# Kernel tuning notes

Hardware: AMD Instinct MI355X
Metric: run time of the kernel (lower is better)

The kernel has to match this reference:

```python
import jax, jax.numpy as jnp
import numpy as np

S, IN_DIM = 16384, 1024
NUM_PROJ, PROJ_DIM, BINS = 100, 64, 20
D = NUM_PROJ * PROJ_DIM
EPS = 1e-12  # F.normalize eps


def setup_inputs() -> dict:
    key = jax.random.key(0)
    kx, kw = jax.random.split(key)
    x = jax.random.normal(kx, (S, IN_DIM), dtype=jnp.float32)
    W = jax.random.normal(kw, (D, IN_DIM), dtype=jnp.float32)  # nn.Linear weight, std=1.0 init
    # mins/maxs as produced by cal_min_max over the data (per projected dim)
    proj = x @ W.T
    mins = jnp.min(proj, axis=0)
    maxs = jnp.max(proj, axis=0)
    return {"x": x, "W": W, "mins": mins, "maxs": maxs,
            "num_of_projection": NUM_PROJ, "bins": BINS}


def reference(x, W, mins, maxs, num_of_projection, bins):
    # get_global_feature(x, normalize=True), all histograms fused via scatter-add
    proj = x @ W.T                                   # [S, D]
    d = proj.shape[1]
    proj_dim = d // num_of_projection
    width = maxs - mins                              # [D]
    # torch.histc semantics: values in [min, max] counted; value == max -> last bin
    idx = jnp.floor((proj - mins) / width * bins).astype(jnp.int32)
    idx = jnp.clip(idx, 0, bins - 1)
    valid = (proj >= mins) & (proj <= maxs)
    flat = idx + jnp.arange(d, dtype=jnp.int32)[None, :] * bins   # [S, D]
    hist = jnp.zeros(d * bins, dtype=proj.dtype).at[flat.reshape(-1)].add(
        valid.reshape(-1).astype(proj.dtype))
    gv = hist.reshape(num_of_projection, proj_dim, bins)
    # F.normalize(p=2, dim=2)
    norm = jnp.linalg.norm(gv, axis=2, keepdims=True)
    gv = gv / jnp.maximum(norm, EPS)
    return gv
```

## Files before the change

### kernel.cpp

```cpp
#include <hip/hip_runtime.h>
#include <cmath>

#define S_DIM 16384
#define K_DIM 1024
#define D_DIM 6400
#define NBINS 20
#define HSTRIDE 21

using half_t = _Float16;
using half8  = __attribute__((ext_vector_type(8))) _Float16;
using f32x4  = __attribute__((ext_vector_type(4))) float;

__global__ void cvt_f32_f16(const float* __restrict__ a, half_t* __restrict__ da, int n8a,
                            const float* __restrict__ b, half_t* __restrict__ db, int n8b,
                            float4* __restrict__ z, int nz4) {
  int i = blockIdx.x * blockDim.x + threadIdx.x;
  if (i < nz4) z[i] = (float4){0.f, 0.f, 0.f, 0.f};
  const float* s; half_t* d; int idx;
  if (i < n8a) { s = a; d = da; idx = i; }
  else { idx = i - n8a; if (idx >= n8b) return; s = b; d = db; }
  float4 v0 = ((const float4*)s)[idx * 2];
  float4 v1 = ((const float4*)s)[idx * 2 + 1];
  half8 h = { (half_t)v0.x, (half_t)v0.y, (half_t)v0.z, (half_t)v0.w,
              (half_t)v1.x, (half_t)v1.y, (half_t)v1.z, (half_t)v1.w };
  ((half8*)d)[idx] = h;
}

#define VMWAIT(N) __asm__ volatile("s_waitcnt vmcnt(" #N ")" ::: "memory")
#define BAR()     __asm__ volatile("s_barrier" ::: "memory")
#define SP1()     __builtin_amdgcn_s_setprio(1)
#define SP0()     __builtin_amdgcn_s_setprio(0)

#define GLL(SRC, DST) __builtin_amdgcn_global_load_lds(                      \
    (const __attribute__((address_space(1))) void*)(SRC),                    \
    (__attribute__((address_space(3))) void*)(DST), 16, 0, 0)

__global__ __launch_bounds__(512, 2) void gemm_hist256(
    const half_t* __restrict__ xh, const half_t* __restrict__ wh,
    const float* __restrict__ mins, const float* __restrict__ maxs,
    int* __restrict__ ghist)
{
  __shared__ __align__(16) char ldsA[65536];
  __shared__ __align__(16) char ldsB[65536];
  __shared__ int shist[256 * HSTRIDE];

  const int t    = threadIdx.x;
  const int lane = t & 63;
  const int wv   = t >> 6;
  const int wm   = wv >> 2;
  const int wn   = wv & 3;
  const int l16  = lane & 15;
  const int quad = lane >> 4;

  const int bid = blockIdx.x;
  const int wg  = (bid & 7) * 200 + (bid >> 3);
  const int ct  = wg / 64;
  const int rt  = wg - ct * 64;
  const int colBase = ct * 256;
  const int rowBase = rt * 256;

  for (int i = t; i < 256 * HSTRIDE; i += 512) shist[i] = 0;

  const char* pA[2];
  const char* pB[2];
#pragma unroll
  for (int ks = 0; ks < 2; ++ks) {
    int ch = ((ks * 4 + quad) ^ (lane & 7)) * 16;
    pA[ks] = ldsA + (wm * 128 + l16) * 128 + ch;
    pB[ks] = ldsB + (wn * 64 + l16) * 128 + ch;
  }

  const int r0 = t >> 3;
  const int gOff = r0 * K_DIM + (((t & 7) ^ (r0 & 7)) * 8);
  const int wvD  = wv * 1024;

  const half_t* aS = xh + (size_t)rowBase * K_DIM + gOff;
  const half_t* bS = wh + (size_t)colBase * K_DIM + gOff;

#define STA(PB) {                                                            \
    GLL(aS,                 ldsA + (PB) + wvD);                              \
    GLL(aS +  64 * K_DIM,   ldsA + (PB) +  8192 + wvD);                      \
    GLL(aS + 128 * K_DIM,   ldsA + (PB) + 16384 + wvD);                      \
    GLL(aS + 192 * K_DIM,   ldsA + (PB) + 24576 + wvD);                      \
    aS += 64; }
#define STB(PB) {                                                            \
    GLL(bS,                 ldsB + (PB) + wvD);                              \
    GLL(bS +  64 * K_DIM,   ldsB + (PB) +  8192 + wvD);                      \
    GLL(bS + 128 * K_DIM,   ldsB + (PB) + 16384 + wvD);                      \
    GLL(bS + 192 * K_DIM,   ldsB + (PB) + 24576 + wvD);                      \
    bS += 64; }

  f32x4 acc[8][4];
#pragma unroll
  for (int m = 0; m < 8; ++m)
#pragma unroll
    for (int n = 0; n < 4; ++n) acc[m][n] = (f32x4){0.f, 0.f, 0.f, 0.f};

  half8 aLo[4][2], aHi[4][2], B0[2][2], B1[2][2];

#define LD_ALO(PB)                                                           \
  _Pragma("unroll") for (int fm = 0; fm < 4; ++fm)                           \
  _Pragma("unroll") for (int ks = 0; ks < 2; ++ks)                           \
    aLo[fm][ks] = *(const half8*)(pA[ks] + (PB) + fm * 2048);
#define LD_AHI(PB)                                                           \
  _Pragma("unroll") for (int fm = 0; fm < 4; ++fm)                           \
  _Pragma("unroll") for (int ks = 0; ks < 2; ++ks)                           \
    aHi[fm][ks] = *(const half8*)(pA[ks] + (PB) + 8192 + fm * 2048);
#define LD_B(REG, FNB, PB)                                                   \
  _Pragma("unroll") for (int fn = 0; fn < 2; ++fn)                           \
  _Pragma("unroll") for (int ks = 0; ks < 2; ++ks)                           \
    REG[fn][ks] = *(const half8*)(pB[ks] + (PB) + ((FNB) + fn) * 2048);
#define MQ(AH, BH, MOFF, NOFF)                                               \
  _Pragma("unroll") for (int fm = 0; fm < 4; ++fm)                           \
  _Pragma("unroll") for (int fn = 0; fn < 2; ++fn)                           \
  _Pragma("unroll") for (int ks = 0; ks < 2; ++ks)                           \
    acc[(MOFF) + fm][(NOFF) + fn] = __builtin_amdgcn_mfma_f32_16x16x32_f16(  \
        AH[fm][ks], BH[fn][ks], acc[(MOFF) + fm][(NOFF) + fn], 0, 0, 0);

  STA(0); STB(0); STA(32768); STB(32768);
  VMWAIT(8); BAR();
  LD_ALO(0);
  LD_B(B0, 0, 0);

#define TILE(PB, RDA, RDB, STG)                                              \
  {                                                                          \
    LD_B(B1, 2, PB);                             \
    SP1(); MQ(aLo, B0, 0, 0); SP0();             \
    LD_AHI(PB);                                  \
    SP1(); MQ(aLo, B1, 0, 2); SP0();             \
    VMWAIT(4); BAR();                            \
    if (RDA) LD_ALO((PB) ^ 32768);               \
    SP1(); MQ(aHi, B1, 4, 2); SP0();             \
    VMWAIT(0); BAR();                            \
    if (STG) { STA(PB); STB(PB); }               \
    SP1(); MQ(aHi, B0, 4, 0); SP0();             \
    if (RDB) LD_B(B0, 0, (PB) ^ 32768);          \
  }

  for (int tt = 0; tt < 12; tt += 2) {
    TILE(0,     1, 1, 1);
    TILE(32768, 1, 1, 1);
  }
  TILE(0,     1, 1, 1);
  TILE(32768, 1, 1, 1);
  TILE(0,     1, 1, 0);
  TILE(32768, 0, 0, 0);

#pragma unroll
  for (int nf = 0; nf < 4; ++nf) {
    const int lc = wn * 64 + nf * 16 + l16;
    const float a = mins[colBase + lc], b = maxs[colBase + lc];
    const float sc = (float)NBINS / (b - a);
    int* colHist = &shist[lc * HSTRIDE];
#pragma unroll
    for (int mf = 0; mf < 8; ++mf) {
#pragma unroll
      for (int r = 0; r < 4; ++r) {
        float v = acc[mf][nf][r];
        if (v >= a && v <= b) {
          int bin = (int)((v - a) * sc);
          bin = bin > NBINS - 1 ? NBINS - 1 : bin;
          atomicAdd(&colHist[bin], 1);
        }
      }
    }
  }
  __syncthreads();
  for (int i = t; i < 256 * NBINS; i += 512) {
    int col = i / NBINS, bin = i - col * NBINS;
    int v = shist[col * HSTRIDE + bin];
    if (v) atomicAdd(&ghist[colBase * NBINS + i], v);
  }
}

__global__ __launch_bounds__(256) void gemm_hist_fb(
    const float* __restrict__ xf, const float* __restrict__ wf,
    const float* __restrict__ mins, const float* __restrict__ maxs,
    int* __restrict__ ghist)
{
  __shared__ __align__(16) half_t ldsA[4096];
  __shared__ __align__(16) half_t ldsB[4096];
  __shared__ int shist[128 * HSTRIDE];

  const int t     = threadIdx.x;
  const int lane  = t & 63;
  const int wv    = t >> 6;
  const int waveM = wv >> 1;
  const int waveN = wv & 1;
  const int l16   = lane & 15;
  const int quad  = lane >> 4;
  const int colBase = blockIdx.x * 128;

  for (int i = t; i < 128 * HSTRIDE; i += 256) shist[i] = 0;

  float mn[4], mx[4], inv[4];
  int lcol[4];
#pragma unroll
  for (int nt = 0; nt < 4; ++nt) {
    int lc = waveN * 64 + nt * 16 + l16;
    lcol[nt] = lc;
    float a = mins[colBase + lc], b = maxs[colBase + lc];
    mn[nt] = a; mx[nt] = b;
    inv[nt] = (float)NBINS / (b - a);
  }

  int aOff[4], bOff[4];
#pragma unroll
  for (int mt = 0; mt < 4; ++mt) {
    int m = waveM * 64 + mt * 16 + l16;
    aOff[mt] = (m * 4 + (quad ^ ((m >> 1) & 3))) * 8;
  }
#pragma unroll
  for (int nt = 0; nt < 4; ++nt) {
    int n = waveN * 64 + nt * 16 + l16;
    bOff[nt] = (n * 4 + (quad ^ ((n >> 1) & 3))) * 8;
  }

  for (int rt = blockIdx.y; rt < S_DIM / 128; rt += gridDim.y) {
    const int rowBase = rt * 128;
    f32x4 acc[4][4];
#pragma unroll
    for (int mt = 0; mt < 4; ++mt)
#pragma unroll
      for (int nt = 0; nt < 4; ++nt) acc[mt][nt] = (f32x4){0.f, 0.f, 0.f, 0.f};

    for (int kt = 0; kt < K_DIM; kt += 32) {
      __syncthreads();
#pragma unroll
      for (int i = 0; i < 2; ++i) {
        const int seg = t + i * 256;
        const int row = seg >> 2;
        const int kch = (seg & 3) ^ ((row >> 1) & 3);
        const float* ga = xf + (size_t)(rowBase + row) * K_DIM + kt + kch * 8;
        float4 v0 = ((const float4*)ga)[0];
        float4 v1 = ((const float4*)ga)[1];
        half8 h = { (half_t)v0.x, (half_t)v0.y, (half_t)v0.z, (half_t)v0.w,
                    (half_t)v1.x, (half_t)v1.y, (half_t)v1.z, (half_t)v1.w };
        *(half8*)&ldsA[seg * 8] = h;
        const float* gb = wf + (size_t)(colBase + row) * K_DIM + kt + kch * 8;
        float4 u0 = ((const float4*)gb)[0];
        float4 u1 = ((const float4*)gb)[1];
        half8 g = { (half_t)u0.x, (half_t)u0.y, (half_t)u0.z, (half_t)u0.w,
                    (half_t)u1.x, (half_t)u1.y, (half_t)u1.z, (half_t)u1.w };
        *(half8*)&ldsB[seg * 8] = g;
      }
      __syncthreads();
      {
        half8 aFf[4], bFf[4];
#pragma unroll
        for (int mt = 0; mt < 4; ++mt) aFf[mt] = *(const half8*)&ldsA[aOff[mt]];
#pragma unroll
        for (int nt = 0; nt < 4; ++nt) bFf[nt] = *(const half8*)&ldsB[bOff[nt]];
#pragma unroll
        for (int mt = 0; mt < 4; ++mt)
#pragma unroll
          for (int nt = 0; nt < 4; ++nt)
            acc[mt][nt] = __builtin_amdgcn_mfma_f32_16x16x32_f16(
                aFf[mt], bFf[nt], acc[mt][nt], 0, 0, 0);
      }
    }

#pragma unroll
    for (int nt = 0; nt < 4; ++nt) {
      const float a = mn[nt], b = mx[nt], sc = inv[nt];
      int* colHist = &shist[lcol[nt] * HSTRIDE];
#pragma unroll
      for (int mt = 0; mt < 4; ++mt) {
#pragma unroll
        for (int r = 0; r < 4; ++r) {
          float v = acc[mt][nt][r];
          if (v >= a && v <= b) {
            int bin = (int)((v - a) * sc);
            bin = bin > NBINS - 1 ? NBINS - 1 : bin;
            atomicAdd(&colHist[bin], 1);
          }
        }
      }
    }
  }

  __syncthreads();
  for (int i = t; i < 128 * NBINS; i += 256) {
    int col = i / NBINS, bin = i - col * NBINS;
    int v = shist[col * HSTRIDE + bin];
    if (v) atomicAdd(&ghist[colBase * NBINS + i], v);
  }
}

__global__ void normalize_kernel(const int* __restrict__ hist, float* __restrict__ out) {
  int g = blockIdx.x * blockDim.x + threadIdx.x;
  if (g >= D_DIM) return;
  const int base = g * NBINS;
  float v[NBINS];
  float ss = 0.f;
#pragma unroll
  for (int i = 0; i < NBINS; ++i) { v[i] = (float)hist[base + i]; ss += v[i] * v[i]; }
  float sc = 1.0f / fmaxf(sqrtf(ss), 1e-12f);
#pragma unroll
  for (int i = 0; i < NBINS; ++i) out[base + i] = v[i] * sc;
}

extern "C" void kernel_launch(void* const* d_in, const int* in_sizes, int n_in,
                              void* d_out, int out_size, void* d_ws, size_t ws_size,
                              hipStream_t stream) {
  const float* x    = (const float*)d_in[0];
  const float* W    = (const float*)d_in[1];
  const float* mins = (const float*)d_in[2];
  const float* maxs = (const float*)d_in[3];
  float* out = (float*)d_out;

  const size_t xh_elems = (size_t)S_DIM * K_DIM;
  const size_t wh_elems = (size_t)D_DIM * K_DIM;
  const size_t need = (xh_elems + wh_elems) * sizeof(half_t);

  if (ws_size >= need) {
    half_t* xh = (half_t*)d_ws;
    half_t* wh = xh + xh_elems;
    int n8x = (int)(xh_elems / 8), n8w = (int)(wh_elems / 8);
    int tot = n8x + n8w;
    cvt_f32_f16<<<(tot + 255) / 256, 256, 0, stream>>>(
        x, xh, n8x, W, wh, n8w, (float4*)d_out, out_size / 4);
    gemm_hist256<<<dim3(1600), 512, 0, stream>>>(xh, wh, mins, maxs, (int*)d_out);
  } else {
    hipMemsetAsync(d_out, 0, (size_t)out_size * sizeof(float), stream);
    gemm_hist_fb<<<dim3(D_DIM / 128, 64), 256, 0, stream>>>(
        x, W, mins, maxs, (int*)d_out);
  }

  normalize_kernel<<<(D_DIM + 255) / 256, 256, 0, stream>>>((int*)d_out, out);
}
```

Measured before the change: 375.1 us.

## Load B operands directly from global into registers and shrink LDS staging

Reworks the GEMM main loop so the W (B) fragments are read straight from global memory into registers, double-buffered across K-steps, while only the x (A) tile is staged through LDS with a smaller 32-wide K step and a new XOR swizzle. Cutting LDS use from 128KB+ to about 32KB plus histograms is meant to relieve LDS capacity and bandwidth pressure. The shared histogram is also split into four copies, one per lane quad, to reduce atomic contention, and the copies are summed before the global atomics. The trade-offs are more global-load latency exposure on the B path, twice as many barriers per K, and non-coalesced 16-byte row loads from W.

```diff
diff --git a/kernel.cpp b/kernel.cpp
--- a/kernel.cpp
+++ b/kernel.cpp
@@ -6,6 +6,7 @@
 #define D_DIM 6400
 #define NBINS 20
 #define HSTRIDE 21
+#define QSTRIDE 5377
 
 using half_t = _Float16;
 using half8  = __attribute__((ext_vector_type(8))) _Float16;
@@ -27,6 +28,7 @@
 }
 
 #define VMWAIT(N) __asm__ volatile("s_waitcnt vmcnt(" #N ")" ::: "memory")
+#define LGKM0()   __asm__ volatile("s_waitcnt lgkmcnt(0)" ::: "memory")
 #define BAR()     __asm__ volatile("s_barrier" ::: "memory")
 #define SP1()     __builtin_amdgcn_s_setprio(1)
 #define SP0()     __builtin_amdgcn_s_setprio(0)
@@ -40,9 +42,8 @@
     const float* __restrict__ mins, const float* __restrict__ maxs,
     int* __restrict__ ghist)
 {
-  __shared__ __align__(16) char ldsA[65536];
-  __shared__ __align__(16) char ldsB[65536];
-  __shared__ int shist[256 * HSTRIDE];
+  __shared__ __align__(16) char ldsA[2 * 16384];
+  __shared__ int shist4[4 * QSTRIDE];
 
   const int t    = threadIdx.x;
   const int lane = t & 63;
@@ -59,36 +60,20 @@
   const int colBase = ct * 256;
   const int rowBase = rt * 256;
 
-  for (int i = t; i < 256 * HSTRIDE; i += 512) shist[i] = 0;
-
-  const char* pA[2];
-  const char* pB[2];
-#pragma unroll
-  for (int ks = 0; ks < 2; ++ks) {
-    int ch = ((ks * 4 + quad) ^ (lane & 7)) * 16;
-    pA[ks] = ldsA + (wm * 128 + l16) * 128 + ch;
-    pB[ks] = ldsB + (wn * 64 + l16) * 128 + ch;
-  }
-
-  const int r0 = t >> 3;
-  const int gOff = r0 * K_DIM + (((t & 7) ^ (r0 & 7)) * 8);
+  for (int i = t; i < 4 * QSTRIDE; i += 512) shist4[i] = 0;
+
+  const char* pA = ldsA + (wm * 128 + l16) * 64 + ((quad ^ ((l16 >> 1) & 3)) * 16);
+
+  const int r0   = t >> 2;
+  const int gOff = r0 * K_DIM + (((t & 3) ^ ((t >> 3) & 3)) * 8);
   const int wvD  = wv * 1024;
-
-  const half_t* aS = xh + (size_t)rowBase * K_DIM + gOff;
-  const half_t* bS = wh + (size_t)colBase * K_DIM + gOff;
-
-#define STA(PB) {                                                            \
-    GLL(aS,                 ldsA + (PB) + wvD);                              \
-    GLL(aS +  64 * K_DIM,   ldsA + (PB) +  8192 + wvD);                      \
-    GLL(aS + 128 * K_DIM,   ldsA + (PB) + 16384 + wvD);                      \
-    GLL(aS + 192 * K_DIM,   ldsA + (PB) + 24576 + wvD);                      \
-    aS += 64; }
-#define STB(PB) {                                                            \
-    GLL(bS,                 ldsB + (PB) + wvD);                              \
-    GLL(bS +  64 * K_DIM,   ldsB + (PB) +  8192 + wvD);                      \
-    GLL(bS + 128 * K_DIM,   ldsB + (PB) + 16384 + wvD);                      \
-    GLL(bS + 192 * K_DIM,   ldsB + (PB) + 24576 + wvD);                      \
-    bS += 64; }
+  const half_t* xS  = xh + (size_t)rowBase * K_DIM + gOff;
+  const half_t* xS2 = xS + 128 * K_DIM;
+
+  const half_t* wBp[4];
+#pragma unroll
+  for (int fn = 0; fn < 4; ++fn)
+    wBp[fn] = wh + (size_t)(colBase + wn * 64 + fn * 16 + l16) * K_DIM + quad * 8;
 
   f32x4 acc[8][4];
 #pragma unroll
@@ -96,62 +81,64 @@
 #pragma unroll
     for (int n = 0; n < 4; ++n) acc[m][n] = (f32x4){0.f, 0.f, 0.f, 0.f};
 
-  half8 aLo[4][2], aHi[4][2], B0[2][2], B1[2][2];
-
-#define LD_ALO(PB)                                                           \
-  _Pragma("unroll") for (int fm = 0; fm < 4; ++fm)                           \
-  _Pragma("unroll") for (int ks = 0; ks < 2; ++ks)                           \
-    aLo[fm][ks] = *(const half8*)(pA[ks] + (PB) + fm * 2048);
-#define LD_AHI(PB)                                                           \
-  _Pragma("unroll") for (int fm = 0; fm < 4; ++fm)                           \
-  _Pragma("unroll") for (int ks = 0; ks < 2; ++ks)                           \
-    aHi[fm][ks] = *(const half8*)(pA[ks] + (PB) + 8192 + fm * 2048);
-#define LD_B(REG, FNB, PB)                                                   \
-  _Pragma("unroll") for (int fn = 0; fn < 2; ++fn)                           \
-  _Pragma("unroll") for (int ks = 0; ks < 2; ++ks)                           \
-    REG[fn][ks] = *(const half8*)(pB[ks] + (PB) + ((FNB) + fn) * 2048);
-#define MQ(AH, BH, MOFF, NOFF)                                               \
-  _Pragma("unroll") for (int fm = 0; fm < 4; ++fm)                           \
-  _Pragma("unroll") for (int fn = 0; fn < 2; ++fn)                           \
-  _Pragma("unroll") for (int ks = 0; ks < 2; ++ks)                           \
-    acc[(MOFF) + fm][(NOFF) + fn] = __builtin_amdgcn_mfma_f32_16x16x32_f16(  \
-        AH[fm][ks], BH[fn][ks], acc[(MOFF) + fm][(NOFF) + fn], 0, 0, 0);
-
-  STA(0); STB(0); STA(32768); STB(32768);
-  VMWAIT(8); BAR();
-  LD_ALO(0);
-  LD_B(B0, 0, 0);
-
-#define TILE(PB, RDA, RDB, STG)                                              \
+  half8 aF[8], bA[4], bB[4];
+
+#pragma unroll
+  for (int fn = 0; fn < 4; ++fn) bA[fn] = *(const half8*)(wBp[fn]);
+  GLL(xS,       ldsA + wvD);
+  GLL(xS2,      ldsA + 8192 + wvD);
+  GLL(xS + 32,  ldsA + 16384 + wvD);
+  GLL(xS2 + 32, ldsA + 16384 + 8192 + wvD);
+  VMWAIT(2); BAR();
+
+#define TILE(TT, BC, BN_, W0, W1, DOB, DOS)                                  \
   {                                                                          \
-    LD_B(B1, 2, PB);                             \
-    SP1(); MQ(aLo, B0, 0, 0); SP0();             \
-    LD_AHI(PB);                                  \
-    SP1(); MQ(aLo, B1, 0, 2); SP0();             \
-    VMWAIT(4); BAR();                            \
-    if (RDA) LD_ALO((PB) ^ 32768);               \
-    SP1(); MQ(aHi, B1, 4, 2); SP0();             \
-    VMWAIT(0); BAR();                            \
-    if (STG) { STA(PB); STB(PB); }               \
-    SP1(); MQ(aHi, B0, 4, 0); SP0();             \
-    if (RDB) LD_B(B0, 0, (PB) ^ 32768);          \
-  }
-
-  for (int tt = 0; tt < 12; tt += 2) {
-    TILE(0,     1, 1, 1);
-    TILE(32768, 1, 1, 1);
-  }
-  TILE(0,     1, 1, 1);
-  TILE(32768, 1, 1, 1);
-  TILE(0,     1, 1, 0);
-  TILE(32768, 0, 0, 0);
+    W0;                                                                      \
+    if (DOB) {                                                               \
+      _Pragma("unroll") for (int fn = 0; fn < 4; ++fn)                       \
+        BN_[fn] = *(const half8*)(wBp[fn] + ((TT) + 1) * 32);                \
+    }                                                                        \
+    _Pragma("unroll") for (int mf = 0; mf < 8; ++mf)                         \
+      aF[mf] = *(const half8*)(pA + ((TT) & 1) * 16384 + mf * 1024);         \
+    SP1();                                                                   \
+    _Pragma("unroll") for (int mf = 0; mf < 4; ++mf)                         \
+      _Pragma("unroll") for (int fn = 0; fn < 4; ++fn)                       \
+        acc[mf][fn] = __builtin_amdgcn_mfma_f32_16x16x32_f16(                \
+            aF[mf], BC[fn], acc[mf][fn], 0, 0, 0);                           \
+    SP0();                                                                   \
+    LGKM0(); BAR();                                                          \
+    if (DOS) {                                                               \
+      GLL(xS  + ((TT) + 2) * 32, ldsA + ((TT) & 1) * 16384 + wvD);           \
+      GLL(xS2 + ((TT) + 2) * 32, ldsA + ((TT) & 1) * 16384 + 8192 + wvD);    \
+    }                                                                        \
+    SP1();                                                                   \
+    _Pragma("unroll") for (int mf = 4; mf < 8; ++mf)                         \
+      _Pragma("unroll") for (int fn = 0; fn < 4; ++fn)                       \
+        acc[mf][fn] = __builtin_amdgcn_mfma_f32_16x16x32_f16(                \
+            aF[mf], BC[fn], acc[mf][fn], 0, 0, 0);                           \
+    SP0();                                                                   \
+    W1; BAR();                                                               \
+  }
+
+#define PAIR(T0)                                                             \
+  TILE(T0,       bA, bB, VMWAIT(2), VMWAIT(6), 1, 1)                         \
+  TILE((T0) + 1, bB, bA, VMWAIT(2), VMWAIT(6), 1, 1)
+
+  PAIR(0)  PAIR(2)  PAIR(4)  PAIR(6)  PAIR(8)
+  PAIR(10) PAIR(12) PAIR(14) PAIR(16) PAIR(18)
+  PAIR(20) PAIR(22) PAIR(24) PAIR(26) PAIR(28)
+  TILE(30, bA, bB, VMWAIT(2), VMWAIT(4), 1, 0)
+  TILE(31, bB, bA, VMWAIT(0), (void)0,   0, 0)
+
+#undef PAIR
+#undef TILE
 
 #pragma unroll
   for (int nf = 0; nf < 4; ++nf) {
     const int lc = wn * 64 + nf * 16 + l16;
     const float a = mins[colBase + lc], b = maxs[colBase + lc];
     const float sc = (float)NBINS / (b - a);
-    int* colHist = &shist[lc * HSTRIDE];
+    int* colHist = &shist4[quad * QSTRIDE + lc * HSTRIDE];
 #pragma unroll
     for (int mf = 0; mf < 8; ++mf) {
 #pragma unroll
@@ -168,7 +155,9 @@
   __syncthreads();
   for (int i = t; i < 256 * NBINS; i += 512) {
     int col = i / NBINS, bin = i - col * NBINS;
-    int v = shist[col * HSTRIDE + bin];
+    int base = col * HSTRIDE + bin;
+    int v = shist4[base] + shist4[QSTRIDE + base] +
+            shist4[2 * QSTRIDE + base] + shist4[3 * QSTRIDE + base];
     if (v) atomicAdd(&ghist[colBase * NBINS + i], v);
   }
 }
```

After: 497.9 us. +32.7%, slower.
